# Performance work log

Measured on AMD Instinct MI355X. Metric: run time of the kernel, lower is better.

## Reference

```python
import jax, jax.numpy as jnp
import numpy as np
from jax.ops import segment_sum

N = 100000
E = 1600000
D_IN = 64
D_H = 64
D_OUT = 16


def _gcn_norm(edge_index, n_nodes):
    # PyG GCNConv default: add self-loops, symmetric normalization.
    src, dst = edge_index[0], edge_index[1]
    loop = jnp.arange(n_nodes, dtype=edge_index.dtype)
    src = jnp.concatenate([src, loop])
    dst = jnp.concatenate([dst, loop])
    deg = segment_sum(jnp.ones(src.shape[0], dtype=jnp.float32), dst, num_segments=n_nodes)
    dinv = jnp.where(deg > 0, jax.lax.rsqrt(deg), 0.0)
    norm = dinv[src] * dinv[dst]  # [E + N]
    return src, dst, norm


def _gcn_layer(x, W, b, src, dst, norm, n_nodes):
    h = x @ W  # dense transform first (out_channels <= in_channels)
    msg = h[src] * norm[:, None]          # gather + scale  [E+N, out]
    agg = segment_sum(msg, dst, num_segments=n_nodes)  # scatter-add
    return agg + b


def setup_inputs() -> dict:
    key = jax.random.key(0)
    ks = jax.random.split(key, 10)
    x = jax.random.normal(ks[0], (N, D_IN), dtype=jnp.float32)
    edge_index = jax.random.randint(ks[1], (2, E), 0, N, dtype=jnp.int64)

    def glorot(k, fan_in, fan_out):
        lim = np.sqrt(6.0 / (fan_in + fan_out)).astype(np.float32)
        return jax.random.uniform(k, (fan_in, fan_out), jnp.float32, -lim, lim)

    return {
        "x": x,
        "edge_index": edge_index,
        "W1": glorot(ks[2], D_IN, D_H), "b1": jnp.zeros((D_H,), jnp.float32),
        "W2": glorot(ks[3], D_H, D_H), "b2": jnp.zeros((D_H,), jnp.float32),
        "W3": glorot(ks[4], D_H, D_H), "b3": jnp.zeros((D_H,), jnp.float32),
        "W4": glorot(ks[5], D_H, D_OUT), "b4": jnp.zeros((D_OUT,), jnp.float32),
    }


def reference(x, edge_index, W1, b1, W2, b2, W3, b3, W4, b4):
    n = x.shape[0]
    src, dst, norm = _gcn_norm(edge_index, n)
    h = jax.nn.relu(_gcn_layer(x, W1, b1, src, dst, norm, n))
    h = jax.nn.relu(_gcn_layer(h, W2, b2, src, dst, norm, n))
    h = jax.nn.relu(_gcn_layer(h, W3, b3, src, dst, norm, n))
    return _gcn_layer(h, W4, b4, src, dst, norm, n)
```

## Files before the change

### kernel.cpp

```cpp
#include <hip/hip_runtime.h>
#include <hip/hip_fp16.h>

#define NN 100000
#define NE 1600000
#define BK 512
#define BKSH 9
#define NBKT 196
#define SLOT 9216
#define SRCMASK 0x1FFFF

typedef _Float16 half2v __attribute__((ext_vector_type(2)));

__device__ inline float dot2acc(unsigned int a, unsigned int b, float c) {
#if __has_builtin(__builtin_amdgcn_fdot2)
    union { unsigned int u; half2v h; } ua, ub;
    ua.u = a; ub.u = b;
    return __builtin_amdgcn_fdot2(ua.h, ub.h, c, false);
#else
    float2 fa = __half22float2(*(const __half2*)&a);
    float2 fb = __half22float2(*(const __half2*)&b);
    return c + fa.x * fb.x + fa.y * fb.y;
#endif
}

__device__ inline int wave_incl_scan(int v, int lane) {
#pragma unroll
    for (int off = 1; off < 64; off <<= 1) {
        int t = __shfl_up(v, off, 64);
        if (lane >= off) v += t;
    }
    return v;
}


__global__ __launch_bounds__(1024) void bscatter_kernel(const int* __restrict__ src,
                                                        const int* __restrict__ dst,
                                                        int* __restrict__ bcur,
                                                        unsigned int* __restrict__ bedges,
                                                        int e) {
    __shared__ int h[256];
    __shared__ int sc[256];
    __shared__ int gb[256];
    __shared__ int2 stg[8192];
    int tid = threadIdx.x;
    int tile = blockIdx.x * 8192;
    int cnt_tile = min(8192, e - tile);
    if (tid < 256) h[tid] = 0;
    __syncthreads();
    unsigned int pk[8]; int rk[8], bk[8];
#pragma unroll
    for (int j = 0; j < 8; j++) {
        int li = tid + j * 1024;
        if (li < cnt_tile) {
            int s = src[tile + li];
            int d = dst[tile + li];
            bk[j] = d >> BKSH;
            pk[j] = ((unsigned)(d & (BK - 1)) << 17) | (unsigned)s;
            rk[j] = atomicAdd(&h[bk[j]], 1);
        } else bk[j] = -1;
    }
    __syncthreads();
    if (tid < 64) {
        int b0 = tid * 4;
        int c0 = h[b0], c1 = h[b0 + 1], c2 = h[b0 + 2], c3 = h[b0 + 3];
        int s4 = c0 + c1 + c2 + c3;
        int incl = wave_incl_scan(s4, tid);
        int base = incl - s4;
        sc[b0] = base; sc[b0 + 1] = base + c0;
        sc[b0 + 2] = base + c0 + c1; sc[b0 + 3] = base + c0 + c1 + c2;
        if (c0) gb[b0] = atomicAdd(&bcur[b0], c0);
        if (c1) gb[b0 + 1] = atomicAdd(&bcur[b0 + 1], c1);
        if (c2) gb[b0 + 2] = atomicAdd(&bcur[b0 + 2], c2);
        if (c3) gb[b0 + 3] = atomicAdd(&bcur[b0 + 3], c3);
    }
    __syncthreads();
#pragma unroll
    for (int j = 0; j < 8; j++)
        if (bk[j] >= 0) stg[sc[bk[j]] + rk[j]] = make_int2((int)pk[j], bk[j]);
    __syncthreads();
#pragma unroll
    for (int j = 0; j < 8; j++) {
        int li = tid + j * 1024;
        if (li < cnt_tile) {
            int2 p2 = stg[li];
            int b = p2.y;
            bedges[(size_t)b * SLOT + gb[b] + (li - sc[b])] = (unsigned int)p2.x;
        }
    }
}

__global__ __launch_bounds__(1024) void bfill_kernel(const unsigned int* __restrict__ bedges,
                                                     const int* __restrict__ bcur,
                                                     const float* __restrict__ x,
                                                     int* __restrict__ start,
                                                     int* __restrict__ cnt,
                                                     float* __restrict__ dinv,
                                                     int* __restrict__ csr,
                                                     __half* __restrict__ g) {
    __shared__ int lcnt[BK];
    __shared__ int lstart[BK];
    __shared__ int lcur[BK];
    __shared__ unsigned int sbuf[SLOT];
    int q = blockIdx.x, tid = threadIdx.x;
    size_t ebase = (size_t)q * SLOT;
    int ec = bcur[q];
    int nbase = q * BK;
    if (tid < BK) lcnt[tid] = 0;
    __syncthreads();
    unsigned int pk[9];
#pragma unroll
    for (int k = 0; k < 9; k++) {
        int i = tid + k * 1024;
        pk[k] = (i < ec) ? __builtin_nontemporal_load(&bedges[ebase + i]) : 0xFFFFFFFFu;
    }
#pragma unroll
    for (int k = 0; k < 9; k++)
        if (pk[k] != 0xFFFFFFFFu) atomicAdd(&lcnt[pk[k] >> 17], 1);
    __syncthreads();
    if (tid < 64) {
        int b0 = tid * 8;
        int c[8]; int s = 0;
#pragma unroll
        for (int k = 0; k < 8; k++) { c[k] = lcnt[b0 + k]; s += c[k]; }
        int incl = wave_incl_scan(s, tid);
        int run = incl - s;
#pragma unroll
        for (int k = 0; k < 8; k++) { lstart[b0 + k] = run; lcur[b0 + k] = run; run += c[k]; }
    }
    __syncthreads();
    if (tid < BK) {
        int nd = nbase + tid;
        if (nd < NN) {
            start[nd] = (int)ebase + lstart[tid];
            cnt[nd]   = lcnt[tid];
            dinv[nd]  = rsqrtf((float)lcnt[tid] + 1.0f);
        }
    }
#pragma unroll
    for (int k = 0; k < 9; k++) {
        if (pk[k] != 0xFFFFFFFFu) {
            int r = atomicAdd(&lcur[pk[k] >> 17], 1);
            sbuf[r] = pk[k] & SRCMASK;
        }
    }
    __syncthreads();
    for (int i = tid; i < ec; i += 1024)
        csr[ebase + i] = (int)sbuf[i];
    int nh = NN - nbase; if (nh > BK) nh = BK;
    for (int i = tid; i < nh * 16; i += 1024) {
        int r = i >> 4, c4 = (i & 15) << 2;
        float dvv = rsqrtf((float)lcnt[r] + 1.0f);
        size_t off = (size_t)(nbase + r) * 64 + c4;
        float4 v = *(const float4*)&x[off];
        union { __half2 h[2]; uint2 u; } pq;
        pq.h[0] = __floats2half2_rn(v.x * dvv, v.y * dvv);
        pq.h[1] = __floats2half2_rn(v.z * dvv, v.w * dvv);
        *(uint2*)&g[off] = pq.u;
    }
}

template<int LAST>
__global__ __launch_bounds__(512) void fused_layer_kernel(const __half* __restrict__ g,
                                                          const int* __restrict__ csr,
                                                          const int* __restrict__ start,
                                                          const int* __restrict__ cnt,
                                                          const float* __restrict__ dinv,
                                                          const float* __restrict__ Wg,
                                                          const float* __restrict__ bias,
                                                          const float* __restrict__ W4,
                                                          __half* __restrict__ gout,
                                                          __half* __restrict__ s4out, int n) {
    __shared__ uint4 wpk[8][64];
    __shared__ __half zh[8][64];
    __shared__ __half z2[8][64];
    __shared__ uint4 w4pk[8][16];
    __shared__ float bs[64];
    int tid = threadIdx.x;
    {
        int p = tid >> 6, c = tid & 63;
        float w[8];
#pragma unroll
        for (int i = 0; i < 8; i++) w[i] = Wg[(8 * p + i) * 64 + c];
        union { __half2 h; unsigned int u; } u0, u1, u2, u3;
        u0.h = __floats2half2_rn(w[0], w[1]);
        u1.h = __floats2half2_rn(w[2], w[3]);
        u2.h = __floats2half2_rn(w[4], w[5]);
        u3.h = __floats2half2_rn(w[6], w[7]);
        wpk[p][c] = make_uint4(u0.u, u1.u, u2.u, u3.u);
    }
    if (LAST && tid < 128) {
        int p = tid >> 4, j = tid & 15;
        float w[8];
#pragma unroll
        for (int i = 0; i < 8; i++) w[i] = W4[(8 * p + i) * 16 + j];
        union { __half2 h; unsigned int u; } u0, u1, u2, u3;
        u0.h = __floats2half2_rn(w[0], w[1]);
        u1.h = __floats2half2_rn(w[2], w[3]);
        u2.h = __floats2half2_rn(w[4], w[5]);
        u3.h = __floats2half2_rn(w[6], w[7]);
        w4pk[p][j] = make_uint4(u0.u, u1.u, u2.u, u3.u);
    }
    if (tid < 64) bs[tid] = bias[tid];
    __syncthreads();

    int wv = tid >> 6, lane = tid & 63;
    int node = blockIdx.x * 8 + wv;
    float acc = 0.f;
    float dv = 0.f;
    if (node < n) {
        int st = __builtin_amdgcn_readfirstlane(start[node]);
        int cn = __builtin_amdgcn_readfirstlane(cnt[node]);
        dv = dinv[node];
        acc = __half2float(g[(size_t)node * 64 + lane]);
        int e = 0;
        for (; e + 7 < cn; e += 8) {
            int u[8]; float a[8];
#pragma unroll
            for (int j = 0; j < 8; j++) u[j] = __builtin_nontemporal_load(&csr[st + e + j]);
#pragma unroll
            for (int j = 0; j < 8; j++) a[j] = __half2float(g[(size_t)u[j] * 64 + lane]);
            acc += ((a[0] + a[1]) + (a[2] + a[3])) + ((a[4] + a[5]) + (a[6] + a[7]));
        }
        for (; e + 3 < cn; e += 4) {
            int u0 = __builtin_nontemporal_load(&csr[st + e + 0]);
            int u1 = __builtin_nontemporal_load(&csr[st + e + 1]);
            int u2 = __builtin_nontemporal_load(&csr[st + e + 2]);
            int u3 = __builtin_nontemporal_load(&csr[st + e + 3]);
            float a0 = __half2float(g[(size_t)u0 * 64 + lane]);
            float a1 = __half2float(g[(size_t)u1 * 64 + lane]);
            float a2 = __half2float(g[(size_t)u2 * 64 + lane]);
            float a3 = __half2float(g[(size_t)u3 * 64 + lane]);
            acc += (a0 + a1) + (a2 + a3);
        }
        for (; e < cn; e++) {
            int u = __builtin_nontemporal_load(&csr[st + e]);
            acc += __half2float(g[(size_t)u * 64 + lane]);
        }
    }
    zh[wv][lane] = __float2half_rn(acc);
    if (node < n) {
        float t = 0.f;
#pragma unroll
        for (int p = 0; p < 8; p++) {
            uint4 wq = wpk[p][lane];
            uint4 zq = *(const uint4*)&zh[wv][p * 8];
            t = dot2acc(zq.x, wq.x, t);
            t = dot2acc(zq.y, wq.y, t);
            t = dot2acc(zq.z, wq.z, t);
            t = dot2acc(zq.w, wq.w, t);
        }
        float o = dv * t + bs[lane];
        o = fmaxf(o, 0.f);
        float g3 = dv * o;
        if (!LAST) {
            gout[(size_t)node * 64 + lane] = __float2half_rn(g3);
        } else {
            z2[wv][lane] = __float2half_rn(g3);
            int col = lane & 15, seg = lane >> 4;
            float t4 = 0.f;
#pragma unroll
            for (int pp = 0; pp < 2; pp++) {
                int p = seg * 2 + pp;
                uint4 wq = w4pk[p][col];
                uint4 zq = *(const uint4*)&z2[wv][p * 8];
                t4 = dot2acc(zq.x, wq.x, t4);
                t4 = dot2acc(zq.y, wq.y, t4);
                t4 = dot2acc(zq.z, wq.z, t4);
                t4 = dot2acc(zq.w, wq.w, t4);
            }
            t4 += __shfl_xor(t4, 16, 64);
            t4 += __shfl_xor(t4, 32, 64);
            if (lane < 16)
                s4out[(size_t)node * 16 + col] = __float2half_rn(t4);
        }
    }
}

__global__ __launch_bounds__(256) void agg16_kernel(const __half* __restrict__ s,
                                                    const int* __restrict__ csr,
                                                    const int* __restrict__ start,
                                                    const int* __restrict__ cnt,
                                                    const float* __restrict__ dinv,
                                                    const float* __restrict__ bias,
                                                    float* __restrict__ out, int n) {
    constexpr int D = 16;
    int tid = threadIdx.x;
    int lane = tid & 63;
    int wave = tid >> 6;
    int col = lane % D;
    int grp = lane / D;
    int node = (blockIdx.x * 4 + wave) * 4 + grp;
    if (node >= n) return;
    int st = start[node];
    int cn = cnt[node];
    float acc = __half2float(s[(size_t)node * D + col]);
    int e = 0;
    for (; e + 7 < cn; e += 8) {
        int u[8]; float a[8];
#pragma unroll
        for (int j = 0; j < 8; j++) u[j] = __builtin_nontemporal_load(&csr[st + e + j]);
#pragma unroll
        for (int j = 0; j < 8; j++) a[j] = __half2float(s[(size_t)u[j] * D + col]);
        acc += ((a[0] + a[1]) + (a[2] + a[3])) + ((a[4] + a[5]) + (a[6] + a[7]));
    }
    for (; e + 3 < cn; e += 4) {
        int u0 = __builtin_nontemporal_load(&csr[st + e + 0]);
        int u1 = __builtin_nontemporal_load(&csr[st + e + 1]);
        int u2 = __builtin_nontemporal_load(&csr[st + e + 2]);
        int u3 = __builtin_nontemporal_load(&csr[st + e + 3]);
        float a0 = __half2float(s[(size_t)u0 * D + col]);
        float a1 = __half2float(s[(size_t)u1 * D + col]);
        float a2 = __half2float(s[(size_t)u2 * D + col]);
        float a3 = __half2float(s[(size_t)u3 * D + col]);
        acc += (a0 + a1) + (a2 + a3);
    }
    for (; e < cn; e++) {
        int u = __builtin_nontemporal_load(&csr[st + e]);
        acc += __half2float(s[(size_t)u * D + col]);
    }
    float o = dinv[node] * acc + bias[col];
    __builtin_nontemporal_store(o, out + (size_t)node * D + col);
}


extern "C" void kernel_launch(void* const* d_in, const int* in_sizes, int n_in,
                              void* d_out, int out_size, void* d_ws, size_t ws_size,
                              hipStream_t stream) {
    const float* x  = (const float*)d_in[0];
    const int* ei   = (const int*)d_in[1];
    const float* W1 = (const float*)d_in[2];
    const float* b1 = (const float*)d_in[3];
    const float* W2 = (const float*)d_in[4];
    const float* b2 = (const float*)d_in[5];
    const float* W3 = (const float*)d_in[6];
    const float* b3 = (const float*)d_in[7];
    const float* W4 = (const float*)d_in[8];
    const float* b4 = (const float*)d_in[9];
    const int* src = ei;
    const int* dst = ei + NE;

    char* w = (char*)d_ws;
    float* dinv  = (float*)w;          w += (size_t)NN * 4;
    int* cnt     = (int*)w;            w += (size_t)NN * 4;
    int* start   = (int*)w;            w += (size_t)NN * 4;
    int* bcur    = (int*)w;            w += (size_t)256 * 4;
    int* csr     = (int*)w;            w += (size_t)NBKT * SLOT * 4;
    __half* gA   = (__half*)w;         w += (size_t)NN * 64 * 2;
    __half* gB   = (__half*)w;         w += (size_t)NN * 64 * 2;
    __half* s4   = (__half*)w;         w += (size_t)NN * 16 * 2;
    unsigned int* bedges = (unsigned int*)w;  w += (size_t)NBKT * SLOT * 4;

    hipMemsetAsync(bcur, 0, 256 * sizeof(int), stream);
    bscatter_kernel<<<(NE + 8191) / 8192, 1024, 0, stream>>>(src, dst, bcur, bedges, NE);
    bfill_kernel<<<NBKT, 1024, 0, stream>>>(bedges, bcur, x, start, cnt, dinv, csr, gA);

    const int FB = (NN + 7) / 8;
    fused_layer_kernel<0><<<FB, 512, 0, stream>>>(gA, csr, start, cnt, dinv, W1, b1, W4, gB, s4, NN);
    fused_layer_kernel<0><<<FB, 512, 0, stream>>>(gB, csr, start, cnt, dinv, W2, b2, W4, gA, s4, NN);
    fused_layer_kernel<1><<<FB, 512, 0, stream>>>(gA, csr, start, cnt, dinv, W3, b3, W4, gB, s4, NN);

    const int AB16 = (NN + 15) / 16;
    agg16_kernel<<<AB16, 256, 0, stream>>>(s4, csr, start, cnt, dinv, b4, (float*)d_out, NN);
}
```

Before: 310.0 us.

## Replace two-pass bucketed CSR build with histogram, scan, and atomic scatter

The CSR construction changes. The old shared-memory bucket sort (block scatter into 196 buckets, then a per-bucket fill) is replaced by three kernels: a global atomic degree histogram, a block scan that hands out offsets with a global atomic, and an atomic-cursor scatter of source indices into a compact CSR array. The intent is to avoid the intermediate bucket buffer and its extra read/write pass. The cost is many global atomics on random destinations, and the order of neighbours inside each row is no longer deterministic. It also relies on the scan blocks allocating offsets in any order, which still gives correct disjoint ranges.

```diff
diff --git a/kernel.cpp b/kernel.cpp
--- a/kernel.cpp
+++ b/kernel.cpp
@@ -3,11 +3,6 @@
 
 #define NN 100000
 #define NE 1600000
-#define BK 512
-#define BKSH 9
-#define NBKT 196
-#define SLOT 9216
-#define SRCMASK 0x1FFFF
 
 typedef _Float16 half2v __attribute__((ext_vector_type(2)));
 
@@ -33,124 +28,71 @@
 }
 
 
-__global__ __launch_bounds__(1024) void bscatter_kernel(const int* __restrict__ src,
-                                                        const int* __restrict__ dst,
-                                                        int* __restrict__ bcur,
-                                                        unsigned int* __restrict__ bedges,
-                                                        int e) {
-    __shared__ int h[256];
-    __shared__ int sc[256];
-    __shared__ int gb[256];
-    __shared__ int2 stg[8192];
+__global__ __launch_bounds__(256) void hist_kernel(const int* __restrict__ dst,
+                                                   int* __restrict__ cnt, int e) {
+    int i = (blockIdx.x * 256 + threadIdx.x) * 4;
+    if (i + 3 < e) {
+        int4 d = *(const int4*)&dst[i];
+        atomicAdd(&cnt[d.x], 1);
+        atomicAdd(&cnt[d.y], 1);
+        atomicAdd(&cnt[d.z], 1);
+        atomicAdd(&cnt[d.w], 1);
+    } else {
+        for (; i < e; i++) atomicAdd(&cnt[dst[i]], 1);
+    }
+}
+
+__global__ __launch_bounds__(1024) void scan_kernel(const int* __restrict__ cnt,
+                                                    int* __restrict__ start,
+                                                    int* __restrict__ cur,
+                                                    float* __restrict__ dinv,
+                                                    int* __restrict__ alloc) {
+    __shared__ int wsum[16];
+    __shared__ int gbase;
     int tid = threadIdx.x;
-    int tile = blockIdx.x * 8192;
-    int cnt_tile = min(8192, e - tile);
-    if (tid < 256) h[tid] = 0;
+    int node = blockIdx.x * 1024 + tid;
+    int c = (node < NN) ? cnt[node] : 0;
+    int lane = tid & 63, wv = tid >> 6;
+    int incl = wave_incl_scan(c, lane);
+    if (lane == 63) wsum[wv] = incl;
     __syncthreads();
-    unsigned int pk[8]; int rk[8], bk[8];
-#pragma unroll
-    for (int j = 0; j < 8; j++) {
-        int li = tid + j * 1024;
-        if (li < cnt_tile) {
-            int s = src[tile + li];
-            int d = dst[tile + li];
-            bk[j] = d >> BKSH;
-            pk[j] = ((unsigned)(d & (BK - 1)) << 17) | (unsigned)s;
-            rk[j] = atomicAdd(&h[bk[j]], 1);
-        } else bk[j] = -1;
+    if (wv == 0) {
+        int s = (lane < 16) ? wsum[lane] : 0;
+        int incl2 = wave_incl_scan(s, lane);
+        int tot = __shfl(incl2, 15, 64);
+        if (lane == 0) gbase = atomicAdd(alloc, tot);
+        if (lane < 16) wsum[lane] = incl2 - s;
     }
     __syncthreads();
-    if (tid < 64) {
-        int b0 = tid * 4;
-        int c0 = h[b0], c1 = h[b0 + 1], c2 = h[b0 + 2], c3 = h[b0 + 3];
-        int s4 = c0 + c1 + c2 + c3;
-        int incl = wave_incl_scan(s4, tid);
-        int base = incl - s4;
-        sc[b0] = base; sc[b0 + 1] = base + c0;
-        sc[b0 + 2] = base + c0 + c1; sc[b0 + 3] = base + c0 + c1 + c2;
-        if (c0) gb[b0] = atomicAdd(&bcur[b0], c0);
-        if (c1) gb[b0 + 1] = atomicAdd(&bcur[b0 + 1], c1);
-        if (c2) gb[b0 + 2] = atomicAdd(&bcur[b0 + 2], c2);
-        if (c3) gb[b0 + 3] = atomicAdd(&bcur[b0 + 3], c3);
-    }
-    __syncthreads();
-#pragma unroll
-    for (int j = 0; j < 8; j++)
-        if (bk[j] >= 0) stg[sc[bk[j]] + rk[j]] = make_int2((int)pk[j], bk[j]);
-    __syncthreads();
-#pragma unroll
-    for (int j = 0; j < 8; j++) {
-        int li = tid + j * 1024;
-        if (li < cnt_tile) {
-            int2 p2 = stg[li];
-            int b = p2.y;
-            bedges[(size_t)b * SLOT + gb[b] + (li - sc[b])] = (unsigned int)p2.x;
-        }
-    }
-}
-
-__global__ __launch_bounds__(1024) void bfill_kernel(const unsigned int* __restrict__ bedges,
-                                                     const int* __restrict__ bcur,
-                                                     const float* __restrict__ x,
-                                                     int* __restrict__ start,
-                                                     int* __restrict__ cnt,
-                                                     float* __restrict__ dinv,
-                                                     int* __restrict__ csr,
-                                                     __half* __restrict__ g) {
-    __shared__ int lcnt[BK];
-    __shared__ int lstart[BK];
-    __shared__ int lcur[BK];
-    __shared__ unsigned int sbuf[SLOT];
-    int q = blockIdx.x, tid = threadIdx.x;
-    size_t ebase = (size_t)q * SLOT;
-    int ec = bcur[q];
-    int nbase = q * BK;
-    if (tid < BK) lcnt[tid] = 0;
-    __syncthreads();
-    unsigned int pk[9];
-#pragma unroll
-    for (int k = 0; k < 9; k++) {
-        int i = tid + k * 1024;
-        pk[k] = (i < ec) ? __builtin_nontemporal_load(&bedges[ebase + i]) : 0xFFFFFFFFu;
-    }
-#pragma unroll
-    for (int k = 0; k < 9; k++)
-        if (pk[k] != 0xFFFFFFFFu) atomicAdd(&lcnt[pk[k] >> 17], 1);
-    __syncthreads();
-    if (tid < 64) {
-        int b0 = tid * 8;
-        int c[8]; int s = 0;
-#pragma unroll
-        for (int k = 0; k < 8; k++) { c[k] = lcnt[b0 + k]; s += c[k]; }
-        int incl = wave_incl_scan(s, tid);
-        int run = incl - s;
-#pragma unroll
-        for (int k = 0; k < 8; k++) { lstart[b0 + k] = run; lcur[b0 + k] = run; run += c[k]; }
-    }
-    __syncthreads();
-    if (tid < BK) {
-        int nd = nbase + tid;
-        if (nd < NN) {
-            start[nd] = (int)ebase + lstart[tid];
-            cnt[nd]   = lcnt[tid];
-            dinv[nd]  = rsqrtf((float)lcnt[tid] + 1.0f);
-        }
-    }
-#pragma unroll
-    for (int k = 0; k < 9; k++) {
-        if (pk[k] != 0xFFFFFFFFu) {
-            int r = atomicAdd(&lcur[pk[k] >> 17], 1);
-            sbuf[r] = pk[k] & SRCMASK;
-        }
-    }
-    __syncthreads();
-    for (int i = tid; i < ec; i += 1024)
-        csr[ebase + i] = (int)sbuf[i];
-    int nh = NN - nbase; if (nh > BK) nh = BK;
-    for (int i = tid; i < nh * 16; i += 1024) {
+    if (node < NN) {
+        int base = gbase + wsum[wv] + (incl - c);
+        start[node] = base;
+        cur[node]   = base;
+        dinv[node]  = rsqrtf((float)c + 1.0f);
+    }
+}
+
+__global__ __launch_bounds__(256) void scatter_kernel(const int* __restrict__ src,
+                                                      const int* __restrict__ dst,
+                                                      int* __restrict__ cur,
+                                                      int* __restrict__ csr,
+                                                      const float* __restrict__ dinv,
+                                                      const float* __restrict__ x,
+                                                      __half* __restrict__ g, int e) {
+    int stride = gridDim.x * 256;
+    int t0 = blockIdx.x * 256 + threadIdx.x;
+    for (int i = t0 * 4; i < e; i += stride * 4) {
+        int4 s4v = *(const int4*)&src[i];
+        int4 d4v = *(const int4*)&dst[i];
+        csr[atomicAdd(&cur[d4v.x], 1)] = s4v.x;
+        csr[atomicAdd(&cur[d4v.y], 1)] = s4v.y;
+        csr[atomicAdd(&cur[d4v.z], 1)] = s4v.z;
+        csr[atomicAdd(&cur[d4v.w], 1)] = s4v.w;
+    }
+    for (int i = t0; i < NN * 16; i += stride) {
         int r = i >> 4, c4 = (i & 15) << 2;
-        float dvv = rsqrtf((float)lcnt[r] + 1.0f);
-        size_t off = (size_t)(nbase + r) * 64 + c4;
+        float dvv = dinv[r];
+        size_t off = (size_t)r * 64 + c4;
         float4 v = *(const float4*)&x[off];
         union { __half2 h[2]; uint2 u; } pq;
         pq.h[0] = __floats2half2_rn(v.x * dvv, v.y * dvv);
@@ -342,17 +284,19 @@
     char* w = (char*)d_ws;
     float* dinv  = (float*)w;          w += (size_t)NN * 4;
     int* cnt     = (int*)w;            w += (size_t)NN * 4;
+    int* alloc   = (int*)w;            w += 16;
     int* start   = (int*)w;            w += (size_t)NN * 4;
-    int* bcur    = (int*)w;            w += (size_t)256 * 4;
-    int* csr     = (int*)w;            w += (size_t)NBKT * SLOT * 4;
+    int* cur     = (int*)w;            w += (size_t)NN * 4;
+    int* csr     = (int*)w;            w += (size_t)NE * 4;
     __half* gA   = (__half*)w;         w += (size_t)NN * 64 * 2;
     __half* gB   = (__half*)w;         w += (size_t)NN * 64 * 2;
     __half* s4   = (__half*)w;         w += (size_t)NN * 16 * 2;
-    unsigned int* bedges = (unsigned int*)w;  w += (size_t)NBKT * SLOT * 4;
-
-    hipMemsetAsync(bcur, 0, 256 * sizeof(int), stream);
-    bscatter_kernel<<<(NE + 8191) / 8192, 1024, 0, stream>>>(src, dst, bcur, bedges, NE);
-    bfill_kernel<<<NBKT, 1024, 0, stream>>>(bedges, bcur, x, start, cnt, dinv, csr, gA);
+
+    hipMemsetAsync(cnt, 0, (size_t)NN * 4 + 16, stream);
+
+    hist_kernel<<<(NE / 4 + 255) / 256, 256, 0, stream>>>(dst, cnt, NE);
+    scan_kernel<<<(NN + 1023) / 1024, 1024, 0, stream>>>(cnt, start, cur, dinv, alloc);
+    scatter_kernel<<<2048, 256, 0, stream>>>(src, dst, cur, csr, dinv, x, gA, NE);
 
     const int FB = (NN + 7) / 8;
     fused_layer_kernel<0><<<FB, 512, 0, stream>>>(gA, csr, start, cnt, dinv, W1, b1, W4, gB, s4, NN);
```

New measurement: 470.4 us. 51.7% more time.
